# Performance work log

Measured on AMD Instinct MI355X. Metric: run time of the kernel, lower is better.

## Reference

```python
import jax, jax.numpy as jnp
import numpy as np

LENGTHSCALES = np.array([0.1, 0.2, 0.5, 1.0, 2.0, 5.0, 10.0, 20.0], dtype=np.float32)
VALUE_DIM = 64
OUTPUT_DIM = 512
NUM_HEADS = len(LENGTHSCALES)


def setup_inputs() -> dict:
    key = jax.random.key(0)
    k1, k2, k3, k4, k5 = jax.random.split(key, 5)
    B, Lq, Lk, D = 4, 2048, 2048, 3
    query_positions = jax.random.normal(k1, (B, Lq, D), dtype=jnp.float32)
    key_positions = jax.random.normal(k2, (B, Lk, D), dtype=jnp.float32)
    values = jax.random.normal(k3, (B, Lk, NUM_HEADS, VALUE_DIM), dtype=jnp.float32)
    masked_elements = jax.random.randint(k4, (B, Lk), 0, 2) > 0
    # nn.Linear(value_dim*num_heads, output_dim, bias=False): weight [out, in]
    fan_in = VALUE_DIM * NUM_HEADS
    w_out = jax.random.uniform(k5, (OUTPUT_DIM, fan_in), dtype=jnp.float32,
                               minval=-1.0, maxval=1.0) / jnp.sqrt(fan_in)
    lengthscales = jnp.asarray(LENGTHSCALES)
    return {"query_positions": query_positions, "key_positions": key_positions,
            "values": values, "masked_elements": masked_elements,
            "lengthscales": lengthscales, "w_out": w_out}


def reference(query_positions, key_positions, values, masked_elements, lengthscales, w_out):
    # Euclidean distances via mm-trick (matches torch.cdist use_mm_for_euclid_dist)
    q2 = jnp.sum(query_positions ** 2, axis=-1)            # [B, Lq]
    k2 = jnp.sum(key_positions ** 2, axis=-1)              # [B, Lk]
    qk = jnp.einsum('bqd,bkd->bqk', query_positions, key_positions)
    d2 = jnp.maximum(q2[:, :, None] + k2[:, None, :] - 2.0 * qk, 0.0)
    distances = jnp.sqrt(d2)                               # [B, Lq, Lk]
    # per-head scaling + gaussian basis: exp(-(d/ls)^2)
    scaled = distances[:, None, :, :] / lengthscales[None, :, None, None]  # [B, H, Lq, Lk]
    scores = jnp.exp(-(scaled ** 2))
    scores = jnp.where(masked_elements[:, None, None, :], 0.0, scores)
    # masked sum-normalization
    scores = scores / (jnp.sum(jnp.abs(scores), axis=-1, keepdims=True) + 1e-5)
    # attend: values [B, Lk, H, V] -> [B, H, Lk, V]; then flatten heads -> [B, Lq, H*V]
    attended = jnp.einsum('bhqk,bkhv->bqhv', scores, values)
    B, Lq = attended.shape[0], attended.shape[1]
    flat = attended.reshape(B, Lq, -1)
    return flat @ w_out.T                                   # [B, Lq, output_dim]
```

## Files before the change

### kernel.cpp

```cpp
#include <hip/hip_runtime.h>
#include <math.h>

#define BB 4
#define LQ 2048
#define LK 2048
#define HD 8
#define VD 64
#define HV 512
#define SP 72

typedef __attribute__((ext_vector_type(8))) short bf16x8;
typedef __attribute__((ext_vector_type(4))) float f32x4;

static __device__ __forceinline__ unsigned short f2bf(float f) {
    unsigned u = __builtin_bit_cast(unsigned, f);
    unsigned r = (u + 0x7fffu + ((u >> 16) & 1u)) >> 16;
    return (unsigned short)r;
}

static __device__ __forceinline__ float fast_exp2(float x) {
#if __has_builtin(__builtin_amdgcn_exp2f)
    return __builtin_amdgcn_exp2f(x);
#else
    return __expf(x * 0.69314718f);
#endif
}

static __device__ __forceinline__ unsigned pack_trunc(float even, float odd) {
    return __builtin_amdgcn_perm(__builtin_bit_cast(unsigned, odd),
                                 __builtin_bit_cast(unsigned, even), 0x07060302u);
}

__global__ __launch_bounds__(256) void cvt_vals(
    const float* __restrict__ vals, unsigned short* __restrict__ vals_t)
{
    __shared__ unsigned short st[64 * SP];
    const int tid = threadIdx.x;
    const int kt = blockIdx.x, h = blockIdx.y, b = blockIdx.z;

    const int k  = tid >> 2;
    const int vb = (tid & 3) * 16;
    const float* src = vals + (((size_t)(b * LK + kt * 64 + k) * HD + h)) * VD + vb;
    float4 f0 = *(const float4*)(src);
    float4 f1 = *(const float4*)(src + 4);
    float4 f2 = *(const float4*)(src + 8);
    float4 f3 = *(const float4*)(src + 12);
    const float fv[16] = {f0.x,f0.y,f0.z,f0.w, f1.x,f1.y,f1.z,f1.w,
                          f2.x,f2.y,f2.z,f2.w, f3.x,f3.y,f3.z,f3.w};
#pragma unroll
    for (int j = 0; j < 16; ++j) st[(vb + j) * SP + k] = f2bf(fv[j]);
    __syncthreads();

    const int v  = tid >> 2;
    const int kb = (tid & 3) * 16;
    uint4 o0 = *(const uint4*)&st[v * SP + kb];
    uint4 o1 = *(const uint4*)&st[v * SP + kb + 8];
    unsigned short* dst = vals_t + ((size_t)((b * HD + h) * VD + v)) * LK + kt * 64 + kb;
    *(uint4*)dst       = o0;
    *(uint4*)(dst + 8) = o1;
}

__global__ __launch_bounds__(256) void cvt_w(
    const float* __restrict__ w, unsigned short* __restrict__ wb)
{
    const int i = (blockIdx.x * 256 + threadIdx.x) * 4;
    float4 f = *(const float4*)(w + i);
    ushort4 o;
    o.x = f2bf(f.x); o.y = f2bf(f.y); o.z = f2bf(f.z); o.w = f2bf(f.w);
    *(ushort4*)(wb + i) = o;
}

__global__ __launch_bounds__(256, 1) void attend3(
    const float* __restrict__ qpos,
    const float* __restrict__ kpos,
    const unsigned short* __restrict__ vals_t,
    const int*   __restrict__ kmask,
    const float* __restrict__ ls,
    unsigned short* __restrict__ attended)
{
    __shared__ __align__(16) unsigned short sV[2][256 * SP];
    __shared__ __align__(16) float skx[2][64], sky[2][64], skz[2][64];

    const int tid  = threadIdx.x;
    const int qt = blockIdx.x, hs = blockIdx.y, b = blockIdx.z;
    const int q0 = qt * 64;
    const int wave = tid >> 6, lane = tid & 63;
    const int ln = lane & 15, kq = lane >> 4;
    const int h = hs * 4 + wave;

    const float lsh = ls[h];
    const float ch  = -1.44269504f / (lsh * lsh);

    float qx[4], qy[4], qz[4];
#pragma unroll
    for (int qs = 0; qs < 4; ++qs) {
        const float* qp = qpos + (size_t)(b * LQ + q0 + qs * 16 + ln) * 3;
        qx[qs] = qp[0]; qy[qs] = qp[1]; qz[qs] = qp[2];
    }

    const unsigned short* vsrc = vals_t + (size_t)((b * HD + h) * VD + lane) * LK;

    uint4 vreg[8];
    float kxr = 0.f, kyr = 0.f, kzr = 0.f;
#pragma unroll
    for (int j = 0; j < 8; ++j) vreg[j] = ((const uint4*)vsrc)[j];
    if (tid < 64) {
        const int idx = b * LK + tid;
        kxr = kpos[(size_t)idx * 3];
        kyr = kpos[(size_t)idx * 3 + 1];
        kzr = kpos[(size_t)idx * 3 + 2];
        if (kmask[idx]) kxr = 3.0e37f;
    }
    {
        unsigned short* d = &sV[0][tid * SP];
#pragma unroll
        for (int j = 0; j < 8; ++j) *(uint4*)(d + j * 8) = vreg[j];
        if (tid < 64) { skx[0][tid] = kxr; sky[0][tid] = kyr; skz[0][tid] = kzr; }
    }
    __syncthreads();

    f32x4 acc[4][4];
#pragma unroll
    for (int i = 0; i < 4; ++i)
#pragma unroll
        for (int j = 0; j < 4; ++j) acc[i][j] = (f32x4){0.f, 0.f, 0.f, 0.f};
    float pden[4] = {0.f, 0.f, 0.f, 0.f};

    for (int t = 0; t < 32; ++t) {
        const int cur = t & 1;
        const int tn  = (t < 31) ? t + 1 : 0;

        {
            const unsigned short* s = vsrc + tn * 64;
#pragma unroll
            for (int j = 0; j < 8; ++j) vreg[j] = ((const uint4*)s)[j];
        }
        if (tid < 64) {
            const int idx = b * LK + tn * 64 + tid;
            kxr = kpos[(size_t)idx * 3];
            kyr = kpos[(size_t)idx * 3 + 1];
            kzr = kpos[(size_t)idx * 3 + 2];
            if (kmask[idx]) kxr = 3.0e37f;
        }

        bf16x8 bfrag[4][2];
#pragma unroll
        for (int vt = 0; vt < 4; ++vt) {
            const unsigned short* bp = &sV[cur][(wave * 64 + vt * 16 + ln) * SP + kq * 8];
            bfrag[vt][0] = *(const bf16x8*)(bp);
            bfrag[vt][1] = *(const bf16x8*)(bp + 32);
        }

        float kxa[16], kya[16], kza[16];
        *(float4*)&kxa[0]  = *(const float4*)&skx[cur][kq * 8];
        *(float4*)&kxa[4]  = *(const float4*)&skx[cur][kq * 8 + 4];
        *(float4*)&kxa[8]  = *(const float4*)&skx[cur][kq * 8 + 32];
        *(float4*)&kxa[12] = *(const float4*)&skx[cur][kq * 8 + 36];
        *(float4*)&kya[0]  = *(const float4*)&sky[cur][kq * 8];
        *(float4*)&kya[4]  = *(const float4*)&sky[cur][kq * 8 + 4];
        *(float4*)&kya[8]  = *(const float4*)&sky[cur][kq * 8 + 32];
        *(float4*)&kya[12] = *(const float4*)&sky[cur][kq * 8 + 36];
        *(float4*)&kza[0]  = *(const float4*)&skz[cur][kq * 8];
        *(float4*)&kza[4]  = *(const float4*)&skz[cur][kq * 8 + 4];
        *(float4*)&kza[8]  = *(const float4*)&skz[cur][kq * 8 + 32];
        *(float4*)&kza[12] = *(const float4*)&skz[cur][kq * 8 + 36];

#pragma unroll
        for (int qs = 0; qs < 4; ++qs) {
            float s[16];
#pragma unroll
            for (int j = 0; j < 16; ++j) {
                const float dx = qx[qs] - kxa[j];
                const float dy = qy[qs] - kya[j];
                const float dz = qz[qs] - kza[j];
                const float d2 = fmaf(dx, dx, fmaf(dy, dy, dz * dz));
                const float sc = fast_exp2(d2 * ch);
                pden[qs] += sc;
                s[j] = sc;
            }
            unsigned pk[8];
#pragma unroll
            for (int p = 0; p < 8; ++p) pk[p] = pack_trunc(s[2 * p], s[2 * p + 1]);
            const bf16x8 a0 = __builtin_bit_cast(bf16x8, *(uint4*)&pk[0]);
            const bf16x8 a1 = __builtin_bit_cast(bf16x8, *(uint4*)&pk[4]);
#pragma unroll
            for (int vt = 0; vt < 4; ++vt) {
                acc[qs][vt] = __builtin_amdgcn_mfma_f32_16x16x32_bf16(a0, bfrag[vt][0], acc[qs][vt], 0, 0, 0);
                acc[qs][vt] = __builtin_amdgcn_mfma_f32_16x16x32_bf16(a1, bfrag[vt][1], acc[qs][vt], 0, 0, 0);
            }
        }

        {
            const int nb = tn & 1;
            unsigned short* d = &sV[nb][tid * SP];
#pragma unroll
            for (int j = 0; j < 8; ++j) *(uint4*)(d + j * 8) = vreg[j];
            if (tid < 64) { skx[nb][tid] = kxr; sky[nb][tid] = kyr; skz[nb][tid] = kzr; }
        }
        __syncthreads();
    }

    float inv[4];
#pragma unroll
    for (int qs = 0; qs < 4; ++qs) {
        float v = pden[qs];
        v += __shfl_xor(v, 16, 64);
        v += __shfl_xor(v, 32, 64);
        inv[qs] = 1.0f / (v + 1e-5f);
    }
    float ivq[4][4];
#pragma unroll
    for (int qs = 0; qs < 4; ++qs)
#pragma unroll
        for (int r = 0; r < 4; ++r) ivq[qs][r] = __shfl(inv[qs], kq * 4 + r, 64);

#pragma unroll
    for (int qs = 0; qs < 4; ++qs)
#pragma unroll
        for (int vt = 0; vt < 4; ++vt)
#pragma unroll
            for (int r = 0; r < 4; ++r) {
                const int q = q0 + qs * 16 + kq * 4 + r;
                attended[(size_t)(b * LQ + q) * HV + h * VD + vt * 16 + ln] =
                    f2bf(acc[qs][vt][r] * ivq[qs][r]);
            }
}

__global__ __launch_bounds__(256, 1) void proj3(
    const unsigned short* __restrict__ A,
    const unsigned short* __restrict__ Wb,
    float* __restrict__ C)
{
    __shared__ __align__(16) unsigned short sA[128 * SP];
    __shared__ __align__(16) unsigned short sW[128 * SP];

    const int tid = threadIdx.x;
    const int n0 = blockIdx.x * 128, m0 = blockIdx.y * 128;
    const int wave = tid >> 6, lane = tid & 63;
    const int ln = lane & 15, kq = lane >> 4;
    const int mw = (wave >> 1) * 64, nw = (wave & 1) * 64;
    const int sr = tid >> 1, sh = (tid & 1) * 32;

    f32x4 acc[4][4];
#pragma unroll
    for (int i = 0; i < 4; ++i)
#pragma unroll
        for (int j = 0; j < 4; ++j) acc[i][j] = (f32x4){0.f, 0.f, 0.f, 0.f};

    for (int k0 = 0; k0 < 512; k0 += 64) {
        __syncthreads();
        {
            const unsigned short* a = A  + (size_t)(m0 + sr) * 512 + k0 + sh;
            const unsigned short* w = Wb + (size_t)(n0 + sr) * 512 + k0 + sh;
            uint4 a0 = ((const uint4*)a)[0], a1 = ((const uint4*)a)[1],
                  a2 = ((const uint4*)a)[2], a3 = ((const uint4*)a)[3];
            uint4 w0 = ((const uint4*)w)[0], w1 = ((const uint4*)w)[1],
                  w2 = ((const uint4*)w)[2], w3 = ((const uint4*)w)[3];
            unsigned short* da = &sA[sr * SP + sh];
            unsigned short* dw = &sW[sr * SP + sh];
            ((uint4*)da)[0] = a0; ((uint4*)da)[1] = a1;
            *(uint4*)(da + 16) = a2; *(uint4*)(da + 24) = a3;
            ((uint4*)dw)[0] = w0; ((uint4*)dw)[1] = w1;
            *(uint4*)(dw + 16) = w2; *(uint4*)(dw + 24) = w3;
        }
        __syncthreads();

        bf16x8 af[4][2], bf[4][2];
#pragma unroll
        for (int mt = 0; mt < 4; ++mt) {
            const unsigned short* ap = &sA[(mw + mt * 16 + ln) * SP + kq * 8];
            af[mt][0] = *(const bf16x8*)(ap);
            af[mt][1] = *(const bf16x8*)(ap + 32);
        }
#pragma unroll
        for (int nt = 0; nt < 4; ++nt) {
            const unsigned short* bp = &sW[(nw + nt * 16 + ln) * SP + kq * 8];
            bf[nt][0] = *(const bf16x8*)(bp);
            bf[nt][1] = *(const bf16x8*)(bp + 32);
        }
#pragma unroll
        for (int mt = 0; mt < 4; ++mt)
#pragma unroll
            for (int nt = 0; nt < 4; ++nt) {
                acc[mt][nt] = __builtin_amdgcn_mfma_f32_16x16x32_bf16(af[mt][0], bf[nt][0], acc[mt][nt], 0, 0, 0);
                acc[mt][nt] = __builtin_amdgcn_mfma_f32_16x16x32_bf16(af[mt][1], bf[nt][1], acc[mt][nt], 0, 0, 0);
            }
    }

#pragma unroll
    for (int mt = 0; mt < 4; ++mt)
#pragma unroll
        for (int nt = 0; nt < 4; ++nt)
#pragma unroll
            for (int r = 0; r < 4; ++r)
                C[(size_t)(m0 + mw + mt * 16 + kq * 4 + r) * 512 + n0 + nw + nt * 16 + ln] =
                    acc[mt][nt][r];
}

extern "C" void kernel_launch(void* const* d_in, const int* in_sizes, int n_in,
                              void* d_out, int out_size, void* d_ws, size_t ws_size,
                              hipStream_t stream) {
    const float* qpos  = (const float*)d_in[0];
    const float* kpos  = (const float*)d_in[1];
    const float* vals  = (const float*)d_in[2];
    const int*   kmask = (const int*)  d_in[3];
    const float* ls    = (const float*)d_in[4];
    const float* wout  = (const float*)d_in[5];
    float* out = (float*)d_out;

    unsigned short* vals_t   = (unsigned short*)d_ws;
    unsigned short* attended = vals_t + (size_t)4 * 1024 * 1024;
    unsigned short* w_bf     = vals_t + (size_t)8 * 1024 * 1024;

    cvt_vals<<<dim3(32, HD, BB), 256, 0, stream>>>(vals, vals_t);
    cvt_w   <<<dim3(256), 256, 0, stream>>>(wout, w_bf);
    attend3 <<<dim3(32, 2, BB), 256, 0, stream>>>(qpos, kpos, vals_t, kmask, ls, attended);
    proj3   <<<dim3(4, 64), 256, 0, stream>>>(attended, w_bf, out);
}
```

Measured before the change: 189.5 us.

## Restructure attend kernel: per-wave query tiles, direct global loads, XCD-aware block mapping

```diff
diff --git a/kernel.cpp b/kernel.cpp
--- a/kernel.cpp
+++ b/kernel.cpp
@@ -70,7 +70,7 @@
     *(ushort4*)(wb + i) = o;
 }
 
-__global__ __launch_bounds__(256, 1) void attend3(
+__global__ __launch_bounds__(256) void attend4(
     const float* __restrict__ qpos,
     const float* __restrict__ kpos,
     const unsigned short* __restrict__ vals_t,
@@ -78,155 +78,120 @@
     const float* __restrict__ ls,
     unsigned short* __restrict__ attended)
 {
-    __shared__ __align__(16) unsigned short sV[2][256 * SP];
-    __shared__ __align__(16) float skx[2][64], sky[2][64], skz[2][64];
-
-    const int tid  = threadIdx.x;
-    const int qt = blockIdx.x, hs = blockIdx.y, b = blockIdx.z;
-    const int q0 = qt * 64;
+    const int tid = threadIdx.x;
+    const int bi  = blockIdx.x;
+    const int xcd = bi & 7, sub = (bi >> 3) & 3, qc = bi >> 5;
+    const int slice = xcd * 4 + sub;
+    const int b = slice >> 3, h = slice & 7;
     const int wave = tid >> 6, lane = tid & 63;
     const int ln = lane & 15, kq = lane >> 4;
-    const int h = hs * 4 + wave;
 
     const float lsh = ls[h];
     const float ch  = -1.44269504f / (lsh * lsh);
 
-    float qx[4], qy[4], qz[4];
-#pragma unroll
-    for (int qs = 0; qs < 4; ++qs) {
-        const float* qp = qpos + (size_t)(b * LQ + q0 + qs * 16 + ln) * 3;
-        qx[qs] = qp[0]; qy[qs] = qp[1]; qz[qs] = qp[2];
-    }
-
-    const unsigned short* vsrc = vals_t + (size_t)((b * HD + h) * VD + lane) * LK;
-
-    uint4 vreg[8];
-    float kxr = 0.f, kyr = 0.f, kzr = 0.f;
-#pragma unroll
-    for (int j = 0; j < 8; ++j) vreg[j] = ((const uint4*)vsrc)[j];
-    if (tid < 64) {
-        const int idx = b * LK + tid;
-        kxr = kpos[(size_t)idx * 3];
-        kyr = kpos[(size_t)idx * 3 + 1];
-        kzr = kpos[(size_t)idx * 3 + 2];
-        if (kmask[idx]) kxr = 3.0e37f;
-    }
-    {
-        unsigned short* d = &sV[0][tid * SP];
-#pragma unroll
-        for (int j = 0; j < 8; ++j) *(uint4*)(d + j * 8) = vreg[j];
-        if (tid < 64) { skx[0][tid] = kxr; sky[0][tid] = kyr; skz[0][tid] = kzr; }
-    }
-    __syncthreads();
-
-    f32x4 acc[4][4];
-#pragma unroll
-    for (int i = 0; i < 4; ++i)
+    const int qbase = qc * 128 + wave * 32;
+    float qx[2], qy[2], qz[2];
+#pragma unroll
+    for (int st = 0; st < 2; ++st) {
+        const float* qp = qpos + (size_t)(b * LQ + qbase + st * 16 + ln) * 3;
+        qx[st] = qp[0]; qy[st] = qp[1]; qz[st] = qp[2];
+    }
+
+    const unsigned short* vbase = vals_t + (size_t)((b * HD + h) * VD) * LK;
+    const float* kpb = kpos + (size_t)b * LK * 3;
+    const int*   kmb = kmask + b * LK;
+
+    f32x4 acc[2][4];
+#pragma unroll
+    for (int i = 0; i < 2; ++i)
 #pragma unroll
         for (int j = 0; j < 4; ++j) acc[i][j] = (f32x4){0.f, 0.f, 0.f, 0.f};
-    float pden[4] = {0.f, 0.f, 0.f, 0.f};
+    float pden[2] = {0.f, 0.f};
 
     for (int t = 0; t < 32; ++t) {
-        const int cur = t & 1;
-        const int tn  = (t < 31) ? t + 1 : 0;
-
-        {
-            const unsigned short* s = vsrc + tn * 64;
-#pragma unroll
-            for (int j = 0; j < 8; ++j) vreg[j] = ((const uint4*)s)[j];
-        }
-        if (tid < 64) {
-            const int idx = b * LK + tn * 64 + tid;
-            kxr = kpos[(size_t)idx * 3];
-            kyr = kpos[(size_t)idx * 3 + 1];
-            kzr = kpos[(size_t)idx * 3 + 2];
-            if (kmask[idx]) kxr = 3.0e37f;
-        }
-
-        bf16x8 bfrag[4][2];
+        bf16x8 bf0[4], bf1[4];
 #pragma unroll
         for (int vt = 0; vt < 4; ++vt) {
-            const unsigned short* bp = &sV[cur][(wave * 64 + vt * 16 + ln) * SP + kq * 8];
-            bfrag[vt][0] = *(const bf16x8*)(bp);
-            bfrag[vt][1] = *(const bf16x8*)(bp + 32);
-        }
-
-        float kxa[16], kya[16], kza[16];
-        *(float4*)&kxa[0]  = *(const float4*)&skx[cur][kq * 8];
-        *(float4*)&kxa[4]  = *(const float4*)&skx[cur][kq * 8 + 4];
-        *(float4*)&kxa[8]  = *(const float4*)&skx[cur][kq * 8 + 32];
-        *(float4*)&kxa[12] = *(const float4*)&skx[cur][kq * 8 + 36];
-        *(float4*)&kya[0]  = *(const float4*)&sky[cur][kq * 8];
-        *(float4*)&kya[4]  = *(const float4*)&sky[cur][kq * 8 + 4];
-        *(float4*)&kya[8]  = *(const float4*)&sky[cur][kq * 8 + 32];
-        *(float4*)&kya[12] = *(const float4*)&sky[cur][kq * 8 + 36];
-        *(float4*)&kza[0]  = *(const float4*)&skz[cur][kq * 8];
-        *(float4*)&kza[4]  = *(const float4*)&skz[cur][kq * 8 + 4];
-        *(float4*)&kza[8]  = *(const float4*)&skz[cur][kq * 8 + 32];
-        *(float4*)&kza[12] = *(const float4*)&skz[cur][kq * 8 + 36];
-
-#pragma unroll
-        for (int qs = 0; qs < 4; ++qs) {
-            float s[16];
-#pragma unroll
-            for (int j = 0; j < 16; ++j) {
-                const float dx = qx[qs] - kxa[j];
-                const float dy = qy[qs] - kya[j];
-                const float dz = qz[qs] - kza[j];
-                const float d2 = fmaf(dx, dx, fmaf(dy, dy, dz * dz));
-                const float sc = fast_exp2(d2 * ch);
-                pden[qs] += sc;
-                s[j] = sc;
-            }
-            unsigned pk[8];
-#pragma unroll
-            for (int p = 0; p < 8; ++p) pk[p] = pack_trunc(s[2 * p], s[2 * p + 1]);
-            const bf16x8 a0 = __builtin_bit_cast(bf16x8, *(uint4*)&pk[0]);
-            const bf16x8 a1 = __builtin_bit_cast(bf16x8, *(uint4*)&pk[4]);
+            const unsigned short* bp = vbase + (size_t)(vt * 16 + ln) * LK + t * 64 + kq * 8;
+            bf0[vt] = *(const bf16x8*)(bp);
+            bf1[vt] = *(const bf16x8*)(bp + 32);
+        }
+
+        bf16x8 afr[2][2];
+#pragma unroll
+        for (int half = 0; half < 2; ++half) {
+            const int K0 = t * 64 + half * 32 + kq * 8;
+            float4 kc[6];
+            const float* ksrc = kpb + (size_t)K0 * 3;
+#pragma unroll
+            for (int j = 0; j < 6; ++j) kc[j] = ((const float4*)ksrc)[j];
+            int mk[8];
+            *(int4*)&mk[0] = *(const int4*)(kmb + K0);
+            *(int4*)&mk[4] = *(const int4*)(kmb + K0 + 4);
+            const float* kcf = (const float*)kc;
+            float xs[8], ys[8], zs[8];
+#pragma unroll
+            for (int j = 0; j < 8; ++j) {
+                xs[j] = mk[j] ? 3.0e37f : kcf[3 * j];
+                ys[j] = kcf[3 * j + 1];
+                zs[j] = kcf[3 * j + 2];
+            }
+#pragma unroll
+            for (int st = 0; st < 2; ++st) {
+                float s[8];
+#pragma unroll
+                for (int j = 0; j < 8; ++j) {
+                    const float dx = qx[st] - xs[j];
+                    const float dy = qy[st] - ys[j];
+                    const float dz = qz[st] - zs[j];
+                    const float d2 = fmaf(dx, dx, fmaf(dy, dy, dz * dz));
+                    const float sc = fast_exp2(d2 * ch);
+                    pden[st] += sc;
+                    s[j] = sc;
+                }
+                unsigned pk[4];
+#pragma unroll
+                for (int p = 0; p < 4; ++p) pk[p] = pack_trunc(s[2 * p], s[2 * p + 1]);
+                afr[st][half] = __builtin_bit_cast(bf16x8, *(uint4*)pk);
+            }
+        }
+
+#pragma unroll
+        for (int st = 0; st < 2; ++st)
 #pragma unroll
             for (int vt = 0; vt < 4; ++vt) {
-                acc[qs][vt] = __builtin_amdgcn_mfma_f32_16x16x32_bf16(a0, bfrag[vt][0], acc[qs][vt], 0, 0, 0);
-                acc[qs][vt] = __builtin_amdgcn_mfma_f32_16x16x32_bf16(a1, bfrag[vt][1], acc[qs][vt], 0, 0, 0);
-            }
-        }
-
-        {
-            const int nb = tn & 1;
-            unsigned short* d = &sV[nb][tid * SP];
-#pragma unroll
-            for (int j = 0; j < 8; ++j) *(uint4*)(d + j * 8) = vreg[j];
-            if (tid < 64) { skx[nb][tid] = kxr; sky[nb][tid] = kyr; skz[nb][tid] = kzr; }
-        }
-        __syncthreads();
-    }
-
-    float inv[4];
-#pragma unroll
-    for (int qs = 0; qs < 4; ++qs) {
-        float v = pden[qs];
+                acc[st][vt] = __builtin_amdgcn_mfma_f32_16x16x32_bf16(afr[st][0], bf0[vt], acc[st][vt], 0, 0, 0);
+                acc[st][vt] = __builtin_amdgcn_mfma_f32_16x16x32_bf16(afr[st][1], bf1[vt], acc[st][vt], 0, 0, 0);
+            }
+    }
+
+    float inv[2];
+#pragma unroll
+    for (int st = 0; st < 2; ++st) {
+        float v = pden[st];
         v += __shfl_xor(v, 16, 64);
         v += __shfl_xor(v, 32, 64);
-        inv[qs] = 1.0f / (v + 1e-5f);
-    }
-    float ivq[4][4];
-#pragma unroll
-    for (int qs = 0; qs < 4; ++qs)
-#pragma unroll
-        for (int r = 0; r < 4; ++r) ivq[qs][r] = __shfl(inv[qs], kq * 4 + r, 64);
-
-#pragma unroll
-    for (int qs = 0; qs < 4; ++qs)
+        inv[st] = 1.0f / (v + 1e-5f);
+    }
+    float ivq[2][4];
+#pragma unroll
+    for (int st = 0; st < 2; ++st)
+#pragma unroll
+        for (int r = 0; r < 4; ++r) ivq[st][r] = __shfl(inv[st], kq * 4 + r, 64);
+
+#pragma unroll
+    for (int st = 0; st < 2; ++st)
 #pragma unroll
         for (int vt = 0; vt < 4; ++vt)
 #pragma unroll
             for (int r = 0; r < 4; ++r) {
-                const int q = q0 + qs * 16 + kq * 4 + r;
+                const int q = qbase + st * 16 + kq * 4 + r;
                 attended[(size_t)(b * LQ + q) * HV + h * VD + vt * 16 + ln] =
-                    f2bf(acc[qs][vt][r] * ivq[qs][r]);
-            }
-}
-
-__global__ __launch_bounds__(256, 1) void proj3(
+                    f2bf(acc[st][vt][r] * ivq[st][r]);
+            }
+}
+
+__global__ __launch_bounds__(256, 1) void proj4(
     const unsigned short* __restrict__ A,
     const unsigned short* __restrict__ Wb,
     float* __restrict__ C)
@@ -265,7 +230,7 @@
         }
         __syncthreads();
 
-        bf16x8 af[4][2], bf[4][2];
+        bf16x8 af[4][2], bfr[4][2];
 #pragma unroll
         for (int mt = 0; mt < 4; ++mt) {
             const unsigned short* ap = &sA[(mw + mt * 16 + ln) * SP + kq * 8];
@@ -275,15 +240,15 @@
 #pragma unroll
         for (int nt = 0; nt < 4; ++nt) {
             const unsigned short* bp = &sW[(nw + nt * 16 + ln) * SP + kq * 8];
-            bf[nt][0] = *(const bf16x8*)(bp);
-            bf[nt][1] = *(const bf16x8*)(bp + 32);
+            bfr[nt][0] = *(const bf16x8*)(bp);
+            bfr[nt][1] = *(const bf16x8*)(bp + 32);
         }
 #pragma unroll
         for (int mt = 0; mt < 4; ++mt)
 #pragma unroll
             for (int nt = 0; nt < 4; ++nt) {
-                acc[mt][nt] = __builtin_amdgcn_mfma_f32_16x16x32_bf16(af[mt][0], bf[nt][0], acc[mt][nt], 0, 0, 0);
-                acc[mt][nt] = __builtin_amdgcn_mfma_f32_16x16x32_bf16(af[mt][1], bf[nt][1], acc[mt][nt], 0, 0, 0);
+                acc[mt][nt] = __builtin_amdgcn_mfma_f32_16x16x32_bf16(af[mt][0], bfr[nt][0], acc[mt][nt], 0, 0, 0);
+                acc[mt][nt] = __builtin_amdgcn_mfma_f32_16x16x32_bf16(af[mt][1], bfr[nt][1], acc[mt][nt], 0, 0, 0);
             }
     }
 
@@ -314,6 +279,6 @@
 
     cvt_vals<<<dim3(32, HD, BB), 256, 0, stream>>>(vals, vals_t);
     cvt_w   <<<dim3(256), 256, 0, stream>>>(wout, w_bf);
-    attend3 <<<dim3(32, 2, BB), 256, 0, stream>>>(qpos, kpos, vals_t, kmask, ls, attended);
-    proj3   <<<dim3(4, 64), 256, 0, stream>>>(attended, w_bf, out);
-}
+    attend4 <<<dim3(512), 256, 0, stream>>>(qpos, kpos, vals_t, kmask, ls, attended);
+    proj4   <<<dim3(4, 64), 256, 0, stream>>>(attended, w_bf, out);
+}
```

New measurement: 194.0 us. 2.4% more time.
